# Performance work log

Measured on AMD Instinct MI355X. Metric: run time of the kernel, lower is better.

The kernel has to match this reference:

```python
import jax, jax.numpy as jnp
import numpy as np

CUTOFF = 10.0
NUM_GAUSSIANS = 50
LOG2 = float(np.log(2.0))
PI = float(np.pi)


def ssp(v):
    # shifted softplus: softplus(x) - log(2)
    return jax.nn.softplus(v) - LOG2


def setup_inputs() -> dict:
    key = jax.random.key(0)
    ks = jax.random.split(key, 16)
    N, E, H, F, G, L = 10000, 320000, 128, 128, NUM_GAUSSIANS, 6
    s = 0.08  # param scale to keep activations stable over 6 layers
    return {
        "x": jax.random.randint(ks[0], (N,), 0, 100),
        "edge_index": jax.random.randint(ks[1], (2, E), 0, N),
        "edge_dist": jax.random.uniform(ks[2], (E,), jnp.float32) * CUTOFF,
        "emb": jax.random.normal(ks[3], (100, H), jnp.float32) * s,
        "mlp_w1": jax.random.normal(ks[4], (L, G, F), jnp.float32) * s,
        "mlp_b1": jnp.zeros((L, F), jnp.float32),
        "mlp_w2": jax.random.normal(ks[5], (L, F, F), jnp.float32) * s,
        "mlp_b2": jnp.zeros((L, F), jnp.float32),
        "lin1_w": jax.random.normal(ks[6], (L, H, F), jnp.float32) * s,
        "lin2_w": jax.random.normal(ks[7], (L, F, H), jnp.float32) * s,
        "lin2_b": jnp.zeros((L, H), jnp.float32),
        "lin_w": jax.random.normal(ks[8], (L, H, H), jnp.float32) * s,
        "lin_b": jnp.zeros((L, H), jnp.float32),
        "out1_w": jax.random.normal(ks[9], (H, H // 2), jnp.float32) * s,
        "out1_b": jnp.zeros((H // 2,), jnp.float32),
        "out2_w": jax.random.normal(ks[10], (H // 2, H // 2), jnp.float32) * s,
        "out2_b": jnp.zeros((H // 2,), jnp.float32),
        "ro_w": jax.random.normal(ks[11], (H // 2, 12), jnp.float32) * s,
        "ro_b": jnp.zeros((12,), jnp.float32),
    }


def reference(x, edge_index, edge_dist, emb, mlp_w1, mlp_b1, mlp_w2, mlp_b2,
              lin1_w, lin2_w, lin2_b, lin_w, lin_b,
              out1_w, out1_b, out2_w, out2_b, ro_w, ro_b):
    N = x.shape[0]
    L = mlp_w1.shape[0]
    src, dst = edge_index[0], edge_index[1]

    h = emb[x]  # [N, H]

    # Gaussian smearing of distances -> [E, G]
    offset = jnp.linspace(0.0, CUTOFF, NUM_GAUSSIANS)
    coeff = -0.5 / (offset[1] - offset[0]) ** 2
    ea = jnp.exp(coeff * (edge_dist[:, None] - offset[None, :]) ** 2)

    # cosine cutoff envelope C [E]
    C = 0.5 * (jnp.cos(edge_dist * PI / CUTOFF) + 1.0)

    for l in range(L):
        # per-edge filter: MLP(gaussian) * cutoff  -> [E, F]
        W = (ssp(ea @ mlp_w1[l] + mlp_b1[l]) @ mlp_w2[l] + mlp_b2[l]) * C[:, None]
        xf = h @ lin1_w[l]                      # [N, F] (lin1, no bias)
        msg = xf[src] * W                       # gather + elementwise [E, F]
        agg = jax.ops.segment_sum(msg, dst, num_segments=N)  # scatter-add
        conv = agg @ lin2_w[l] + lin2_b[l]      # [N, H]
        h = h + (ssp(conv) @ lin_w[l] + lin_b[l])

    t = ssp(h @ out1_w + out1_b)
    t = t @ out2_w + out2_b
    h_agg = jnp.sum(t, axis=0)                  # [H//2]
    return h_agg @ ro_w + ro_b                  # [12]
```

## Files before the change

### kernel.cpp

```cpp
#include <hip/hip_runtime.h>
#include <math.h>

#define E_NUM 320000
#define N_NUM 10000
#define NB8   (N_NUM / 8)
#define NB16  (N_NUM / 16)
#define TAB   4096

typedef unsigned short ushort_t;
typedef short short8_t __attribute__((ext_vector_type(8)));
typedef float f32x4    __attribute__((ext_vector_type(4)));

#define WP_O1   294912
#define WP_O2   303104
#define WP_W1T  307200
#define WP_W2T  356352
#define WP_TOT  454656

__device__ __forceinline__ float ssp_f(float x) {
    return fmaxf(x, 0.f) + __logf(1.f + __expf(-fabsf(x))) - 0.69314718056f;
}

__device__ __forceinline__ float bf2f(ushort_t u) {
    union { unsigned int i; float f; } v;
    v.i = ((unsigned int)u) << 16;
    return v.f;
}
__device__ __forceinline__ ushort_t f2bf(float f) {
    union { float f; unsigned int i; } v;
    v.f = f;
    unsigned int u = v.i;
    unsigned int r = (u + 0x7FFFu + ((u >> 16) & 1u)) >> 16;
    return (ushort_t)r;
}

__global__ __launch_bounds__(256) void hist_kernel(const int* __restrict__ ei,
                                                   int* __restrict__ counts) {
    int e = blockIdx.x * 256 + threadIdx.x;
    if (e < E_NUM) atomicAdd(&counts[ei[E_NUM + e]], 1);
}

__global__ __launch_bounds__(256) void scan_kernel(const int* __restrict__ counts,
                                                   int* __restrict__ offs,
                                                   int* __restrict__ cursor) {
    __shared__ int part[256];
    const int tid = threadIdx.x;
    const int CH = 40;
    int base = tid * CH;
    int s = 0;
    for (int i = 0; i < CH; ++i) {
        int idx = base + i;
        if (idx < N_NUM) s += counts[idx];
    }
    part[tid] = s;
    __syncthreads();
    for (int off = 1; off < 256; off <<= 1) {
        int v = (tid >= off) ? part[tid - off] : 0;
        __syncthreads();
        part[tid] += v;
        __syncthreads();
    }
    int run = (tid > 0) ? part[tid - 1] : 0;
    for (int i = 0; i < CH; ++i) {
        int idx = base + i;
        if (idx < N_NUM) {
            offs[idx] = run;
            cursor[idx] = run;
            run += counts[idx];
        }
    }
    if (tid == 255) offs[N_NUM] = part[255];
}

__global__ __launch_bounds__(256) void scatter_kernel(const int* __restrict__ ei,
                                                      const float* __restrict__ dist,
                                                      int* __restrict__ cursor,
                                                      int* __restrict__ meta) {
    int e = blockIdx.x * 256 + threadIdx.x;
    if (e >= E_NUM) return;
    int d = ei[E_NUM + e];
    int pos = atomicAdd(&cursor[d], 1);
    float t = dist[e] * ((float)(TAB - 1) / 10.0f);
    int i0 = (int)(t + 0.5f);
    if (i0 > TAB - 1) i0 = TAB - 1;
    meta[pos] = (i0 << 14) | ei[e];
}

__global__ __launch_bounds__(256) void pack_kernel(const float* __restrict__ lin2_w,
                                                   const float* __restrict__ lin_w,
                                                   const float* __restrict__ lin1_w,
                                                   const float* __restrict__ o1w,
                                                   const float* __restrict__ o2w,
                                                   const float* __restrict__ mlp_w1,
                                                   const float* __restrict__ mlp_w2,
                                                   short* __restrict__ wpack) {
    int idx = blockIdx.x * 256 + threadIdx.x;
    const int M128 = 16384;
    if (idx < 18 * M128) {
        int g = idx / M128, r = idx % M128;
        const float* src;
        if (g < 6) src = lin2_w + g * M128;
        else if (g < 12) src = lin_w + (g - 6) * M128;
        else src = lin1_w + (g - 12) * M128;
        int j = r & 7, L = (r >> 3) & 63, ks = (r >> 9) & 3, t = r >> 11;
        int n = t * 16 + (L & 15);
        int k = ks * 32 + (L >> 4) * 8 + j;
        wpack[idx] = (short)f2bf(src[k * 128 + n]);
    } else if (idx < WP_O2) {
        int r = idx - WP_O1;
        int j = r & 7, L = (r >> 3) & 63, ks = (r >> 9) & 3, t = r >> 11;
        int n = t * 16 + (L & 15);
        int k = ks * 32 + (L >> 4) * 8 + j;
        wpack[idx] = (short)f2bf(o1w[k * 64 + n]);
    } else if (idx < WP_W1T) {
        int r = idx - WP_O2;
        int j = r & 7, L = (r >> 3) & 63, ks = (r >> 9) & 1, t = r >> 10;
        int n = t * 16 + (L & 15);
        int k = ks * 32 + (L >> 4) * 8 + j;
        wpack[idx] = (short)f2bf(o2w[k * 64 + n]);
    } else if (idx < WP_W2T) {
        int r2 = idx - WP_W1T;
        int g = r2 / 8192, r = r2 % 8192;
        int j = r & 7, L = (r >> 3) & 63, ks = (r >> 9) & 1, t = r >> 10;
        int n = t * 16 + (L & 15);
        int k = ks * 32 + (L >> 4) * 8 + j;
        float v = (k < 50) ? mlp_w1[g * 6400 + k * 128 + n] : 0.f;
        wpack[idx] = (short)f2bf(v);
    } else if (idx < WP_TOT) {
        int r2 = idx - WP_W2T;
        int g = r2 / M128, r = r2 % M128;
        int j = r & 7, L = (r >> 3) & 63, ks = (r >> 9) & 3, t = r >> 11;
        int n = t * 16 + (L & 15);
        int k = ks * 32 + (L >> 4) * 8 + j;
        wpack[idx] = (short)f2bf(mlp_w2[g * M128 + k * 128 + n]);
    }
}

__global__ __launch_bounds__(512) void table_kernel(const short* __restrict__ w1t,
                                                    const float* __restrict__ mlp_b1,
                                                    const short* __restrict__ w2t,
                                                    const float* __restrict__ mlp_b2,
                                                    ushort_t* __restrict__ tabB) {
    __shared__ short EA[16 * 72];
    __shared__ short HD[16 * 136];
    const int tid = threadIdx.x;
    const int wv = tid >> 6;
    const int lane = tid & 63;
    const int l = blockIdx.x >> 8;
    const int r0 = (blockIdx.x & 255) * 16;
    const float DG = 10.0f / (float)(TAB - 1);
    const float STEP = 10.0f / 49.0f;
    const float COEFF = -0.5f / (STEP * STEP);

    for (int i = tid; i < 16 * 64; i += 512) {
        int r = i >> 6, k = i & 63;
        float v = 0.f;
        if (k < 50) {
            float d = (float)(r0 + r) * DG;
            float t = d - (float)k * STEP;
            v = __expf(COEFF * t * t);
        }
        EA[r * 72 + k] = (short)f2bf(v);
    }
    __syncthreads();

    const int m = lane & 15, q = lane >> 4;

    {
        f32x4 acc = {0.f, 0.f, 0.f, 0.f};
        #pragma unroll
        for (int ks = 0; ks < 2; ++ks) {
            short8_t a = *(const short8_t*)(EA + m * 72 + ks * 32 + q * 8);
            short8_t b = *(const short8_t*)(w1t + l * 8192 + (wv * 2 + ks) * 512 + lane * 8);
            acc = __builtin_amdgcn_mfma_f32_16x16x32_bf16(a, b, acc, 0, 0, 0);
        }
        float bv = mlp_b1[l * 128 + wv * 16 + m];
        #pragma unroll
        for (int i = 0; i < 4; ++i)
            HD[(q * 4 + i) * 136 + wv * 16 + m] = (short)f2bf(ssp_f(acc[i] + bv));
    }
    __syncthreads();

    {
        f32x4 acc = {0.f, 0.f, 0.f, 0.f};
        #pragma unroll
        for (int ks = 0; ks < 4; ++ks) {
            short8_t a = *(const short8_t*)(HD + m * 136 + ks * 32 + q * 8);
            short8_t b = *(const short8_t*)(w2t + l * 16384 + (wv * 4 + ks) * 512 + lane * 8);
            acc = __builtin_amdgcn_mfma_f32_16x16x32_bf16(a, b, acc, 0, 0, 0);
        }
        int col = wv * 16 + m;
        float bv = mlp_b2[l * 128 + col];
        ushort_t* tl = tabB + (size_t)l * TAB * 128;
        #pragma unroll
        for (int i = 0; i < 4; ++i) {
            int row = r0 + q * 4 + i;
            float d = (float)row * DG;
            float C = 0.5f * (__cosf(d * 0.31415926535f) + 1.0f);
            tl[(size_t)row * 128 + col] = f2bf((acc[i] + bv) * C);
        }
    }
}

__device__ __forceinline__ void nacc(ushort4 x, ushort4 t,
                                     float& o0, float& o1, float& o2, float& o3) {
    o0 = fmaf(bf2f(x.x), bf2f(t.x), o0);
    o1 = fmaf(bf2f(x.y), bf2f(t.y), o1);
    o2 = fmaf(bf2f(x.z), bf2f(t.z), o2);
    o3 = fmaf(bf2f(x.w), bf2f(t.w), o3);
}

__global__ __launch_bounds__(256) void embed_lin1_kernel(const int* __restrict__ x,
                                                         const float* __restrict__ emb,
                                                         const float* __restrict__ B,
                                                         float* __restrict__ h,
                                                         ushort_t* __restrict__ xf) {
    __shared__ float AT[128][9];
    __shared__ int s_x[8];
    const int tid = threadIdx.x;
    const int n0 = blockIdx.x * 8;

    if (tid < 8) s_x[tid] = x[n0 + tid];
    __syncthreads();
    for (int i = tid; i < 8 * 128; i += 256) {
        int r = i >> 7, c = i & 127;
        float v = emb[s_x[r] * 128 + c];
        AT[c][r] = v;
        h[(size_t)(n0 + r) * 128 + c] = v;
    }
    __syncthreads();

    const int r  = tid & 7;
    const int c0 = (tid >> 3) * 4;
    float acc[4] = {0.f, 0.f, 0.f, 0.f};
    for (int k = 0; k < 128; k += 4) {
        float a[4];
        #pragma unroll
        for (int u = 0; u < 4; ++u) a[u] = AT[k + u][r];
        #pragma unroll
        for (int u = 0; u < 4; ++u) {
            float4 b = *(const float4*)(B + (size_t)(k + u) * 128 + c0);
            acc[0] = fmaf(a[u], b.x, acc[0]);
            acc[1] = fmaf(a[u], b.y, acc[1]);
            acc[2] = fmaf(a[u], b.z, acc[2]);
            acc[3] = fmaf(a[u], b.w, acc[3]);
        }
    }
    ushort4 o;
    o.x = f2bf(acc[0]); o.y = f2bf(acc[1]); o.z = f2bf(acc[2]); o.w = f2bf(acc[3]);
    *(ushort4*)(xf + (size_t)(n0 + r) * 128 + c0) = o;
}

template <bool LAST>
__global__ __launch_bounds__(512) void layer_kernel(const int* __restrict__ offs,
                                                    const int* __restrict__ meta,
                                                    const ushort_t* __restrict__ xf,
                                                    const ushort_t* __restrict__ tabB,
                                                    const short* __restrict__ w2p,
                                                    const float* __restrict__ lin2_b,
                                                    const short* __restrict__ wlp,
                                                    const float* __restrict__ lin_b,
                                                    const short* __restrict__ w1p,
                                                    float* __restrict__ h,
                                                    ushort_t* __restrict__ xf_out,
                                                    const short* __restrict__ o1p,
                                                    const float* __restrict__ o1b,
                                                    const short* __restrict__ o2p,
                                                    const float* __restrict__ o2b,
                                                    float* __restrict__ gs) {
    __shared__ short A1[16 * 136];
    __shared__ short A2[16 * 136];
    __shared__ float red[4][64];
    const int tid = threadIdx.x;
    const int n0 = blockIdx.x * 16;
    const int wv = tid >> 6;
    const int lane = tid & 63;

    {
        const int half = lane >> 5;
        const int c4 = (lane & 31) * 4;
        const int node = n0 + wv * 2 + half;
        int e   = offs[node];
        int end = offs[node + 1];

        float a0 = 0.f, a1 = 0.f, a2 = 0.f, a3 = 0.f;
        float b0 = 0.f, b1 = 0.f, b2 = 0.f, b3 = 0.f;

        for (; e + 8 <= end; e += 8) {
            int m[8];
            #pragma unroll
            for (int u = 0; u < 8; ++u) m[u] = meta[e + u];
            ushort4 xv[8], tv[8];
            #pragma unroll
            for (int u = 0; u < 8; ++u) {
                xv[u] = *(const ushort4*)(xf + (size_t)(m[u] & 0x3FFF) * 128 + c4);
                tv[u] = *(const ushort4*)(tabB + (size_t)((unsigned)m[u] >> 14) * 128 + c4);
            }
            nacc(xv[0], tv[0], a0, a1, a2, a3);
            nacc(xv[1], tv[1], b0, b1, b2, b3);
            nacc(xv[2], tv[2], a0, a1, a2, a3);
            nacc(xv[3], tv[3], b0, b1, b2, b3);
            nacc(xv[4], tv[4], a0, a1, a2, a3);
            nacc(xv[5], tv[5], b0, b1, b2, b3);
            nacc(xv[6], tv[6], a0, a1, a2, a3);
            nacc(xv[7], tv[7], b0, b1, b2, b3);
        }
        for (; e + 4 <= end; e += 4) {
            int m[4];
            #pragma unroll
            for (int u = 0; u < 4; ++u) m[u] = meta[e + u];
            ushort4 xv[4], tv[4];
            #pragma unroll
            for (int u = 0; u < 4; ++u) {
                xv[u] = *(const ushort4*)(xf + (size_t)(m[u] & 0x3FFF) * 128 + c4);
                tv[u] = *(const ushort4*)(tabB + (size_t)((unsigned)m[u] >> 14) * 128 + c4);
            }
            nacc(xv[0], tv[0], a0, a1, a2, a3);
            nacc(xv[1], tv[1], b0, b1, b2, b3);
            nacc(xv[2], tv[2], a0, a1, a2, a3);
            nacc(xv[3], tv[3], b0, b1, b2, b3);
        }
        for (; e < end; ++e) {
            int mm = meta[e];
            ushort4 xv = *(const ushort4*)(xf + (size_t)(mm & 0x3FFF) * 128 + c4);
            ushort4 tv = *(const ushort4*)(tabB + (size_t)((unsigned)mm >> 14) * 128 + c4);
            nacc(xv, tv, a0, a1, a2, a3);
        }

        unsigned p01 = (unsigned)f2bf(a0 + b0) | ((unsigned)f2bf(a1 + b1) << 16);
        unsigned p23 = (unsigned)f2bf(a2 + b2) | ((unsigned)f2bf(a3 + b3) << 16);
        const int row = wv * 2 + half;
        *(unsigned*)&A1[row * 136 + c4]     = p01;
        *(unsigned*)&A1[row * 136 + c4 + 2] = p23;
    }
    __syncthreads();

    const int m = lane & 15, q = lane >> 4;

    {
        f32x4 acc = {0.f, 0.f, 0.f, 0.f};
        #pragma unroll
        for (int ks = 0; ks < 4; ++ks) {
            short8_t a = *(const short8_t*)(A1 + m * 136 + ks * 32 + q * 8);
            short8_t b = *(const short8_t*)(w2p + (wv * 4 + ks) * 512 + lane * 8);
            acc = __builtin_amdgcn_mfma_f32_16x16x32_bf16(a, b, acc, 0, 0, 0);
        }
        float bv = lin2_b[wv * 16 + m];
        #pragma unroll
        for (int i = 0; i < 4; ++i) {
            int r = q * 4 + i;
            A2[r * 136 + wv * 16 + m] = (short)f2bf(ssp_f(acc[i] + bv));
        }
    }
    __syncthreads();

    {
        f32x4 acc = {0.f, 0.f, 0.f, 0.f};
        #pragma unroll
        for (int ks = 0; ks < 4; ++ks) {
            short8_t a = *(const short8_t*)(A2 + m * 136 + ks * 32 + q * 8);
            short8_t b = *(const short8_t*)(wlp + (wv * 4 + ks) * 512 + lane * 8);
            acc = __builtin_amdgcn_mfma_f32_16x16x32_bf16(a, b, acc, 0, 0, 0);
        }
        float bv = lin_b[wv * 16 + m];
        #pragma unroll
        for (int i = 0; i < 4; ++i) {
            int r = q * 4 + i;
            int grow = n0 + r;
            float h0 = h[(size_t)grow * 128 + wv * 16 + m];
            float hn = h0 + acc[i] + bv;
            if (!LAST) h[(size_t)grow * 128 + wv * 16 + m] = hn;
            A1[r * 136 + wv * 16 + m] = (short)f2bf(hn);
        }
    }
    __syncthreads();

    if constexpr (!LAST) {
        f32x4 acc = {0.f, 0.f, 0.f, 0.f};
        #pragma unroll
        for (int ks = 0; ks < 4; ++ks) {
            short8_t a = *(const short8_t*)(A1 + m * 136 + ks * 32 + q * 8);
            short8_t b = *(const short8_t*)(w1p + (wv * 4 + ks) * 512 + lane * 8);
            acc = __builtin_amdgcn_mfma_f32_16x16x32_bf16(a, b, acc, 0, 0, 0);
        }
        #pragma unroll
        for (int i = 0; i < 4; ++i) {
            int r = q * 4 + i;
            int grow = n0 + r;
            xf_out[(size_t)grow * 128 + wv * 16 + m] = f2bf(acc[i]);
        }
    } else {
        if (wv < 4) {
            f32x4 acc = {0.f, 0.f, 0.f, 0.f};
            #pragma unroll
            for (int ks = 0; ks < 4; ++ks) {
                short8_t a = *(const short8_t*)(A1 + m * 136 + ks * 32 + q * 8);
                short8_t b = *(const short8_t*)(o1p + (wv * 4 + ks) * 512 + lane * 8);
                acc = __builtin_amdgcn_mfma_f32_16x16x32_bf16(a, b, acc, 0, 0, 0);
            }
            float bv = o1b[wv * 16 + m];
            #pragma unroll
            for (int i = 0; i < 4; ++i) {
                int r = q * 4 + i;
                A2[r * 136 + wv * 16 + m] = (short)f2bf(ssp_f(acc[i] + bv));
            }
        }
        __syncthreads();
        if (wv < 4) {
            f32x4 acc = {0.f, 0.f, 0.f, 0.f};
            #pragma unroll
            for (int ks = 0; ks < 2; ++ks) {
                short8_t a = *(const short8_t*)(A2 + m * 136 + ks * 32 + q * 8);
                short8_t b = *(const short8_t*)(o2p + (wv * 2 + ks) * 512 + lane * 8);
                acc = __builtin_amdgcn_mfma_f32_16x16x32_bf16(a, b, acc, 0, 0, 0);
            }
            float bv = o2b[wv * 16 + m];
            float part = acc[0] + acc[1] + acc[2] + acc[3] + 4.0f * bv;
            red[q][wv * 16 + m] = part;
        }
        __syncthreads();
        if (tid < 64) {
            float s = red[0][tid] + red[1][tid] + red[2][tid] + red[3][tid];
            atomicAdd(&gs[tid], s);
        }
    }
}

__global__ void final_kernel(const float* __restrict__ gs,
                             const float* __restrict__ ro_w,
                             const float* __restrict__ ro_b,
                             float* __restrict__ out) {
    int i = threadIdx.x;
    if (i < 12) {
        float s = ro_b[i];
        for (int k = 0; k < 64; ++k) s = fmaf(gs[k], ro_w[k * 12 + i], s);
        out[i] = s;
    }
}

extern "C" void kernel_launch(void* const* d_in, const int* in_sizes, int n_in,
                              void* d_out, int out_size, void* d_ws, size_t ws_size,
                              hipStream_t stream) {
    const int*   x      = (const int*)d_in[0];
    const int*   ei     = (const int*)d_in[1];
    const float* dist   = (const float*)d_in[2];
    const float* emb    = (const float*)d_in[3];
    const float* mlp_w1 = (const float*)d_in[4];
    const float* mlp_b1 = (const float*)d_in[5];
    const float* mlp_w2 = (const float*)d_in[6];
    const float* mlp_b2 = (const float*)d_in[7];
    const float* lin1_w = (const float*)d_in[8];
    const float* lin2_w = (const float*)d_in[9];
    const float* lin2_b = (const float*)d_in[10];
    const float* lin_w  = (const float*)d_in[11];
    const float* lin_b  = (const float*)d_in[12];
    const float* out1_w = (const float*)d_in[13];
    const float* out1_b = (const float*)d_in[14];
    const float* out2_w = (const float*)d_in[15];
    const float* out2_b = (const float*)d_in[16];
    const float* ro_w   = (const float*)d_in[17];
    const float* ro_b   = (const float*)d_in[18];
    float* out = (float*)d_out;

    char* base = (char*)d_ws;
    float*    h     = (float*)base;     base += (size_t)N_NUM * 128 * 4;
    ushort_t* tabB  = (ushort_t*)base;  base += (size_t)6 * TAB * 128 * 2;
    ushort_t* xf0   = (ushort_t*)base;  base += (size_t)N_NUM * 128 * 2;
    ushort_t* xf1   = (ushort_t*)base;  base += (size_t)N_NUM * 128 * 2;
    int*      meta  = (int*)base;       base += (size_t)E_NUM * 4;
    short*    wpack = (short*)base;     base += (size_t)WP_TOT * 2;
    float*    gs    = (float*)base;     base += 64 * 4;
    int*      offs  = (int*)base;       base += (N_NUM + 1) * 4;
    int*      cursor= (int*)base;       base += N_NUM * 4;
    int*      counts= (int*)base;       base += N_NUM * 4;

    hipMemsetAsync(counts, 0, N_NUM * sizeof(int), stream);
    hipMemsetAsync(gs, 0, 64 * sizeof(float), stream);

    hist_kernel<<<(E_NUM + 255) / 256, 256, 0, stream>>>(ei, counts);
    scan_kernel<<<1, 256, 0, stream>>>(counts, offs, cursor);
    scatter_kernel<<<(E_NUM + 255) / 256, 256, 0, stream>>>(ei, dist, cursor, meta);

    pack_kernel<<<(WP_TOT + 255) / 256, 256, 0, stream>>>(
        lin2_w, lin_w, lin1_w, out1_w, out2_w, mlp_w1, mlp_w2, wpack);
    table_kernel<<<6 * (TAB / 16), 512, 0, stream>>>(
        wpack + WP_W1T, mlp_b1, wpack + WP_W2T, mlp_b2, tabB);

    embed_lin1_kernel<<<NB8, 256, 0, stream>>>(x, emb, lin1_w, h, xf0);

    const short* o1p = wpack + WP_O1;
    const short* o2p = wpack + WP_O2;

    for (int l = 0; l < 6; ++l) {
        ushort_t* xin  = (l & 1) ? xf1 : xf0;
        ushort_t* xout = (l & 1) ? xf0 : xf1;
        const ushort_t* tl = tabB + (size_t)l * TAB * 128;
        const short* w2p = wpack + l * 16384;
        const short* wlp = wpack + (6 + l) * 16384;
        if (l < 5) {
            const short* w1p = wpack + (12 + l + 1) * 16384;
            layer_kernel<false><<<NB16, 512, 0, stream>>>(
                offs, meta, xin, tl,
                w2p, lin2_b + l * 128, wlp, lin_b + l * 128, w1p,
                h, xout, nullptr, nullptr, nullptr, nullptr, nullptr);
        } else {
            layer_kernel<true><<<NB16, 512, 0, stream>>>(
                offs, meta, xin, tl,
                w2p, lin2_b + l * 128, wlp, lin_b + l * 128, nullptr,
                h, nullptr, o1p, out1_b, o2p, out2_b, gs);
        }
    }

    final_kernel<<<1, 64, 0, stream>>>(gs, ro_w, ro_b, out);
}
```

Baseline: 352.5 us.

## Halve layer block size, widen gather loads to 16B, shrink filter table

The layer kernel now runs with 256 threads per block. In the gather phase each 16-lane group handles one node with 8-element (16-byte) loads instead of 32 lanes with 4-element loads. Each wave now computes two 16-column tiles in the MFMA stages, so the 4 waves still cover all 128 columns. The filter lookup table is also halved to 2048 distance entries, which reduces table build work and cache footprint but coarsens the distance quantisation, and the meta index encoding must still fit.

```diff
diff --git a/kernel.cpp b/kernel.cpp
--- a/kernel.cpp
+++ b/kernel.cpp
@@ -5,7 +5,7 @@
 #define N_NUM 10000
 #define NB8   (N_NUM / 8)
 #define NB16  (N_NUM / 16)
-#define TAB   4096
+#define TAB   2048
 
 typedef unsigned short ushort_t;
 typedef short short8_t __attribute__((ext_vector_type(8)));
@@ -146,8 +146,8 @@
     const int tid = threadIdx.x;
     const int wv = tid >> 6;
     const int lane = tid & 63;
-    const int l = blockIdx.x >> 8;
-    const int r0 = (blockIdx.x & 255) * 16;
+    const int l = blockIdx.x >> 7;
+    const int r0 = (blockIdx.x & 127) * 16;
     const float DG = 10.0f / (float)(TAB - 1);
     const float STEP = 10.0f / 49.0f;
     const float COEFF = -0.5f / (STEP * STEP);
@@ -202,12 +202,10 @@
     }
 }
 
-__device__ __forceinline__ void nacc(ushort4 x, ushort4 t,
-                                     float& o0, float& o1, float& o2, float& o3) {
-    o0 = fmaf(bf2f(x.x), bf2f(t.x), o0);
-    o1 = fmaf(bf2f(x.y), bf2f(t.y), o1);
-    o2 = fmaf(bf2f(x.z), bf2f(t.z), o2);
-    o3 = fmaf(bf2f(x.w), bf2f(t.w), o3);
+__device__ __forceinline__ void nacc8(short8_t x, short8_t t, float* o) {
+    #pragma unroll
+    for (int j = 0; j < 8; ++j)
+        o[j] = fmaf(bf2f((ushort_t)x[j]), bf2f((ushort_t)t[j]), o[j]);
 }
 
 __global__ __launch_bounds__(256) void embed_lin1_kernel(const int* __restrict__ x,
@@ -251,8 +249,22 @@
     *(ushort4*)(xf + (size_t)(n0 + r) * 128 + c0) = o;
 }
 
+__device__ __forceinline__ void mfma_stage2(const short* A_lds, const short* wp,
+                                            int lane, int t0, int t1,
+                                            f32x4& acc0, f32x4& acc1) {
+    const int m = lane & 15, q = lane >> 4;
+    #pragma unroll
+    for (int ks = 0; ks < 4; ++ks) {
+        short8_t a  = *(const short8_t*)(A_lds + m * 136 + ks * 32 + q * 8);
+        short8_t b0 = *(const short8_t*)(wp + (t0 * 4 + ks) * 512 + lane * 8);
+        short8_t b1 = *(const short8_t*)(wp + (t1 * 4 + ks) * 512 + lane * 8);
+        acc0 = __builtin_amdgcn_mfma_f32_16x16x32_bf16(a, b0, acc0, 0, 0, 0);
+        acc1 = __builtin_amdgcn_mfma_f32_16x16x32_bf16(a, b1, acc1, 0, 0, 0);
+    }
+}
+
 template <bool LAST>
-__global__ __launch_bounds__(512) void layer_kernel(const int* __restrict__ offs,
+__global__ __launch_bounds__(256) void layer_kernel(const int* __restrict__ offs,
                                                     const int* __restrict__ meta,
                                                     const ushort_t* __restrict__ xf,
                                                     const ushort_t* __restrict__ tabB,
@@ -277,120 +289,109 @@
     const int lane = tid & 63;
 
     {
-        const int half = lane >> 5;
-        const int c4 = (lane & 31) * 4;
-        const int node = n0 + wv * 2 + half;
+        const int qt = lane >> 4;
+        const int c8 = (lane & 15) * 8;
+        const int node = n0 + wv * 4 + qt;
         int e   = offs[node];
         int end = offs[node + 1];
 
-        float a0 = 0.f, a1 = 0.f, a2 = 0.f, a3 = 0.f;
-        float b0 = 0.f, b1 = 0.f, b2 = 0.f, b3 = 0.f;
+        float accA[8] = {0.f, 0.f, 0.f, 0.f, 0.f, 0.f, 0.f, 0.f};
+        float accB[8] = {0.f, 0.f, 0.f, 0.f, 0.f, 0.f, 0.f, 0.f};
 
         for (; e + 8 <= end; e += 8) {
             int m[8];
             #pragma unroll
             for (int u = 0; u < 8; ++u) m[u] = meta[e + u];
-            ushort4 xv[8], tv[8];
+            short8_t xv[8], tv[8];
             #pragma unroll
             for (int u = 0; u < 8; ++u) {
-                xv[u] = *(const ushort4*)(xf + (size_t)(m[u] & 0x3FFF) * 128 + c4);
-                tv[u] = *(const ushort4*)(tabB + (size_t)((unsigned)m[u] >> 14) * 128 + c4);
+                xv[u] = *(const short8_t*)(xf + (size_t)(m[u] & 0x3FFF) * 128 + c8);
+                tv[u] = *(const short8_t*)(tabB + (size_t)((unsigned)m[u] >> 14) * 128 + c8);
             }
-            nacc(xv[0], tv[0], a0, a1, a2, a3);
-            nacc(xv[1], tv[1], b0, b1, b2, b3);
-            nacc(xv[2], tv[2], a0, a1, a2, a3);
-            nacc(xv[3], tv[3], b0, b1, b2, b3);
-            nacc(xv[4], tv[4], a0, a1, a2, a3);
-            nacc(xv[5], tv[5], b0, b1, b2, b3);
-            nacc(xv[6], tv[6], a0, a1, a2, a3);
-            nacc(xv[7], tv[7], b0, b1, b2, b3);
+            #pragma unroll
+            for (int u = 0; u < 8; ++u)
+                nacc8(xv[u], tv[u], (u & 1) ? accB : accA);
         }
         for (; e + 4 <= end; e += 4) {
             int m[4];
             #pragma unroll
             for (int u = 0; u < 4; ++u) m[u] = meta[e + u];
-            ushort4 xv[4], tv[4];
+            short8_t xv[4], tv[4];
             #pragma unroll
             for (int u = 0; u < 4; ++u) {
-                xv[u] = *(const ushort4*)(xf + (size_t)(m[u] & 0x3FFF) * 128 + c4);
-                tv[u] = *(const ushort4*)(tabB + (size_t)((unsigned)m[u] >> 14) * 128 + c4);
+                xv[u] = *(const short8_t*)(xf + (size_t)(m[u] & 0x3FFF) * 128 + c8);
+                tv[u] = *(const short8_t*)(tabB + (size_t)((unsigned)m[u] >> 14) * 128 + c8);
             }
-            nacc(xv[0], tv[0], a0, a1, a2, a3);
-            nacc(xv[1], tv[1], b0, b1, b2, b3);
-            nacc(xv[2], tv[2], a0, a1, a2, a3);
-            nacc(xv[3], tv[3], b0, b1, b2, b3);
+            #pragma unroll
+            for (int u = 0; u < 4; ++u)
+                nacc8(xv[u], tv[u], (u & 1) ? accB : accA);
         }
         for (; e < end; ++e) {
             int mm = meta[e];
-            ushort4 xv = *(const ushort4*)(xf + (size_t)(mm & 0x3FFF) * 128 + c4);
-            ushort4 tv = *(const ushort4*)(tabB + (size_t)((unsigned)mm >> 14) * 128 + c4);
-            nacc(xv, tv, a0, a1, a2, a3);
-        }
-
-        unsigned p01 = (unsigned)f2bf(a0 + b0) | ((unsigned)f2bf(a1 + b1) << 16);
-        unsigned p23 = (unsigned)f2bf(a2 + b2) | ((unsigned)f2bf(a3 + b3) << 16);
-        const int row = wv * 2 + half;
-        *(unsigned*)&A1[row * 136 + c4]     = p01;
-        *(unsigned*)&A1[row * 136 + c4 + 2] = p23;
+            short8_t xv = *(const short8_t*)(xf + (size_t)(mm & 0x3FFF) * 128 + c8);
+            short8_t tv = *(const short8_t*)(tabB + (size_t)((unsigned)mm >> 14) * 128 + c8);
+            nacc8(xv, tv, accA);
+        }
+
+        short8_t out;
+        #pragma unroll
+        for (int j = 0; j < 8; ++j) out[j] = (short)f2bf(accA[j] + accB[j]);
+        *(short8_t*)&A1[(wv * 4 + qt) * 136 + c8] = out;
     }
     __syncthreads();
 
     const int m = lane & 15, q = lane >> 4;
+    const int t0 = wv * 2, t1 = wv * 2 + 1;
 
     {
-        f32x4 acc = {0.f, 0.f, 0.f, 0.f};
-        #pragma unroll
-        for (int ks = 0; ks < 4; ++ks) {
-            short8_t a = *(const short8_t*)(A1 + m * 136 + ks * 32 + q * 8);
-            short8_t b = *(const short8_t*)(w2p + (wv * 4 + ks) * 512 + lane * 8);
-            acc = __builtin_amdgcn_mfma_f32_16x16x32_bf16(a, b, acc, 0, 0, 0);
-        }
-        float bv = lin2_b[wv * 16 + m];
+        f32x4 acc0 = {0.f, 0.f, 0.f, 0.f}, acc1 = {0.f, 0.f, 0.f, 0.f};
+        mfma_stage2(A1, w2p, lane, t0, t1, acc0, acc1);
+        float bv0 = lin2_b[t0 * 16 + m];
+        float bv1 = lin2_b[t1 * 16 + m];
         #pragma unroll
         for (int i = 0; i < 4; ++i) {
             int r = q * 4 + i;
-            A2[r * 136 + wv * 16 + m] = (short)f2bf(ssp_f(acc[i] + bv));
+            A2[r * 136 + t0 * 16 + m] = (short)f2bf(ssp_f(acc0[i] + bv0));
+            A2[r * 136 + t1 * 16 + m] = (short)f2bf(ssp_f(acc1[i] + bv1));
         }
     }
     __syncthreads();
 
     {
-        f32x4 acc = {0.f, 0.f, 0.f, 0.f};
-        #pragma unroll
-        for (int ks = 0; ks < 4; ++ks) {
-            short8_t a = *(const short8_t*)(A2 + m * 136 + ks * 32 + q * 8);
-            short8_t b = *(const short8_t*)(wlp + (wv * 4 + ks) * 512 + lane * 8);
-            acc = __builtin_amdgcn_mfma_f32_16x16x32_bf16(a, b, acc, 0, 0, 0);
-        }
-        float bv = lin_b[wv * 16 + m];
+        f32x4 acc0 = {0.f, 0.f, 0.f, 0.f}, acc1 = {0.f, 0.f, 0.f, 0.f};
+        mfma_stage2(A2, wlp, lane, t0, t1, acc0, acc1);
+        float bv0 = lin_b[t0 * 16 + m];
+        float bv1 = lin_b[t1 * 16 + m];
         #pragma unroll
         for (int i = 0; i < 4; ++i) {
             int r = q * 4 + i;
             int grow = n0 + r;
-            float h0 = h[(size_t)grow * 128 + wv * 16 + m];
-            float hn = h0 + acc[i] + bv;
-            if (!LAST) h[(size_t)grow * 128 + wv * 16 + m] = hn;
-            A1[r * 136 + wv * 16 + m] = (short)f2bf(hn);
+            float h0 = h[(size_t)grow * 128 + t0 * 16 + m];
+            float h1 = h[(size_t)grow * 128 + t1 * 16 + m];
+            float hn0 = h0 + acc0[i] + bv0;
+            float hn1 = h1 + acc1[i] + bv1;
+            if (!LAST) {
+                h[(size_t)grow * 128 + t0 * 16 + m] = hn0;
+                h[(size_t)grow * 128 + t1 * 16 + m] = hn1;
+            }
+            A1[r * 136 + t0 * 16 + m] = (short)f2bf(hn0);
+            A1[r * 136 + t1 * 16 + m] = (short)f2bf(hn1);
         }
     }
     __syncthreads();
 
     if constexpr (!LAST) {
-        f32x4 acc = {0.f, 0.f, 0.f, 0.f};
-        #pragma unroll
-        for (int ks = 0; ks < 4; ++ks) {
-            short8_t a = *(const short8_t*)(A1 + m * 136 + ks * 32 + q * 8);
-            short8_t b = *(const short8_t*)(w1p + (wv * 4 + ks) * 512 + lane * 8);
-            acc = __builtin_amdgcn_mfma_f32_16x16x32_bf16(a, b, acc, 0, 0, 0);
-        }
+        f32x4 acc0 = {0.f, 0.f, 0.f, 0.f}, acc1 = {0.f, 0.f, 0.f, 0.f};
+        mfma_stage2(A1, w1p, lane, t0, t1, acc0, acc1);
         #pragma unroll
         for (int i = 0; i < 4; ++i) {
             int r = q * 4 + i;
             int grow = n0 + r;
-            xf_out[(size_t)grow * 128 + wv * 16 + m] = f2bf(acc[i]);
+            xf_out[(size_t)grow * 128 + t0 * 16 + m] = f2bf(acc0[i]);
+            xf_out[(size_t)grow * 128 + t1 * 16 + m] = f2bf(acc1[i]);
         }
     } else {
-        if (wv < 4) {
+        {
             f32x4 acc = {0.f, 0.f, 0.f, 0.f};
             #pragma unroll
             for (int ks = 0; ks < 4; ++ks) {
@@ -406,7 +407,7 @@
             }
         }
         __syncthreads();
-        if (wv < 4) {
+        {
             f32x4 acc = {0.f, 0.f, 0.f, 0.f};
             #pragma unroll
             for (int ks = 0; ks < 2; ++ks) {
@@ -499,12 +500,12 @@
         const short* wlp = wpack + (6 + l) * 16384;
         if (l < 5) {
             const short* w1p = wpack + (12 + l + 1) * 16384;
-            layer_kernel<false><<<NB16, 512, 0, stream>>>(
+            layer_kernel<false><<<NB16, 256, 0, stream>>>(
                 offs, meta, xin, tl,
                 w2p, lin2_b + l * 128, wlp, lin_b + l * 128, w1p,
                 h, xout, nullptr, nullptr, nullptr, nullptr, nullptr);
         } else {
-            layer_kernel<true><<<NB16, 512, 0, stream>>>(
+            layer_kernel<true><<<NB16, 256, 0, stream>>>(
                 offs, meta, xin, tl,
                 w2p, lin2_b + l * 128, wlp, lin_b + l * 128, nullptr,
                 h, nullptr, o1p, out1_b, o2p, out2_b, gs);
```

Result: faster. 320.4 us, median of 2 (-9.1%).

## Split each node's edges across two 16-lane groups with 16-byte gathers

Applied to the files above, without the earlier changes.

The edge aggregation now assigns four nodes' halves per wave. Each 16-lane group loads 8 bf16 values per lane (16-byte loads) over half of a node's edge range, and the two partial sums are combined through a shared-memory float buffer. This doubles the independent gather streams per wave and widens each load, which should raise memory-level parallelism in the latency-bound gather. The cost is an extra LDS buffer and an extra synchronisation. Separately, the distance lookup table is halved from 4096 to 2048 entries, which coarsens the filter resolution but shrinks the table's cache footprint and halves the table-building work.

```diff
diff --git a/kernel.cpp b/kernel.cpp
--- a/kernel.cpp
+++ b/kernel.cpp
@@ -5,7 +5,7 @@
 #define N_NUM 10000
 #define NB8   (N_NUM / 8)
 #define NB16  (N_NUM / 16)
-#define TAB   4096
+#define TAB   2048
 
 typedef unsigned short ushort_t;
 typedef short short8_t __attribute__((ext_vector_type(8)));
@@ -146,8 +146,8 @@
     const int tid = threadIdx.x;
     const int wv = tid >> 6;
     const int lane = tid & 63;
-    const int l = blockIdx.x >> 8;
-    const int r0 = (blockIdx.x & 255) * 16;
+    const int l = blockIdx.x >> 7;
+    const int r0 = (blockIdx.x & 127) * 16;
     const float DG = 10.0f / (float)(TAB - 1);
     const float STEP = 10.0f / 49.0f;
     const float COEFF = -0.5f / (STEP * STEP);
@@ -202,12 +202,10 @@
     }
 }
 
-__device__ __forceinline__ void nacc(ushort4 x, ushort4 t,
-                                     float& o0, float& o1, float& o2, float& o3) {
-    o0 = fmaf(bf2f(x.x), bf2f(t.x), o0);
-    o1 = fmaf(bf2f(x.y), bf2f(t.y), o1);
-    o2 = fmaf(bf2f(x.z), bf2f(t.z), o2);
-    o3 = fmaf(bf2f(x.w), bf2f(t.w), o3);
+__device__ __forceinline__ void nacc8(short8_t x, short8_t t, float* o) {
+    #pragma unroll
+    for (int j = 0; j < 8; ++j)
+        o[j] = fmaf(bf2f((ushort_t)x[j]), bf2f((ushort_t)t[j]), o[j]);
 }
 
 __global__ __launch_bounds__(256) void embed_lin1_kernel(const int* __restrict__ x,
@@ -270,6 +268,7 @@
                                                     float* __restrict__ gs) {
     __shared__ short A1[16 * 136];
     __shared__ short A2[16 * 136];
+    __shared__ float PF[32][132];
     __shared__ float red[4][64];
     const int tid = threadIdx.x;
     const int n0 = blockIdx.x * 16;
@@ -277,61 +276,67 @@
     const int lane = tid & 63;
 
     {
-        const int half = lane >> 5;
-        const int c4 = (lane & 31) * 4;
-        const int node = n0 + wv * 2 + half;
-        int e   = offs[node];
-        int end = offs[node + 1];
-
-        float a0 = 0.f, a1 = 0.f, a2 = 0.f, a3 = 0.f;
-        float b0 = 0.f, b1 = 0.f, b2 = 0.f, b3 = 0.f;
-
-        for (; e + 8 <= end; e += 8) {
+        const int qt = lane >> 4;
+        const int c8 = (lane & 15) * 8;
+        const int s = wv * 4 + qt;
+        const int node = n0 + (s >> 1);
+        const int half = s & 1;
+        int beg = offs[node], end = offs[node + 1];
+        int mid = beg + ((end - beg) >> 1);
+        int e    = half ? mid : beg;
+        int stop = half ? end : mid;
+
+        float accA[8] = {0.f, 0.f, 0.f, 0.f, 0.f, 0.f, 0.f, 0.f};
+        float accB[8] = {0.f, 0.f, 0.f, 0.f, 0.f, 0.f, 0.f, 0.f};
+
+        for (; e + 8 <= stop; e += 8) {
             int m[8];
             #pragma unroll
             for (int u = 0; u < 8; ++u) m[u] = meta[e + u];
-            ushort4 xv[8], tv[8];
+            short8_t xv[8], tv[8];
             #pragma unroll
             for (int u = 0; u < 8; ++u) {
-                xv[u] = *(const ushort4*)(xf + (size_t)(m[u] & 0x3FFF) * 128 + c4);
-                tv[u] = *(const ushort4*)(tabB + (size_t)((unsigned)m[u] >> 14) * 128 + c4);
+                xv[u] = *(const short8_t*)(xf + (size_t)(m[u] & 0x3FFF) * 128 + c8);
+                tv[u] = *(const short8_t*)(tabB + (size_t)((unsigned)m[u] >> 14) * 128 + c8);
             }
-            nacc(xv[0], tv[0], a0, a1, a2, a3);
-            nacc(xv[1], tv[1], b0, b1, b2, b3);
-            nacc(xv[2], tv[2], a0, a1, a2, a3);
-            nacc(xv[3], tv[3], b0, b1, b2, b3);
-            nacc(xv[4], tv[4], a0, a1, a2, a3);
-            nacc(xv[5], tv[5], b0, b1, b2, b3);
-            nacc(xv[6], tv[6], a0, a1, a2, a3);
-            nacc(xv[7], tv[7], b0, b1, b2, b3);
-        }
-        for (; e + 4 <= end; e += 4) {
+            #pragma unroll
+            for (int u = 0; u < 8; ++u)
+                nacc8(xv[u], tv[u], (u & 1) ? accB : accA);
+        }
+        for (; e + 4 <= stop; e += 4) {
             int m[4];
             #pragma unroll
             for (int u = 0; u < 4; ++u) m[u] = meta[e + u];
-            ushort4 xv[4], tv[4];
+            short8_t xv[4], tv[4];
             #pragma unroll
             for (int u = 0; u < 4; ++u) {
-                xv[u] = *(const ushort4*)(xf + (size_t)(m[u] & 0x3FFF) * 128 + c4);
-                tv[u] = *(const ushort4*)(tabB + (size_t)((unsigned)m[u] >> 14) * 128 + c4);
+                xv[u] = *(const short8_t*)(xf + (size_t)(m[u] & 0x3FFF) * 128 + c8);
+                tv[u] = *(const short8_t*)(tabB + (size_t)((unsigned)m[u] >> 14) * 128 + c8);
             }
-            nacc(xv[0], tv[0], a0, a1, a2, a3);
-            nacc(xv[1], tv[1], b0, b1, b2, b3);
-            nacc(xv[2], tv[2], a0, a1, a2, a3);
-            nacc(xv[3], tv[3], b0, b1, b2, b3);
-        }
-        for (; e < end; ++e) {
+            #pragma unroll
+            for (int u = 0; u < 4; ++u)
+                nacc8(xv[u], tv[u], (u & 1) ? accB : accA);
+        }
+        for (; e < stop; ++e) {
             int mm = meta[e];
-            ushort4 xv = *(const ushort4*)(xf + (size_t)(mm & 0x3FFF) * 128 + c4);
-            ushort4 tv = *(const ushort4*)(tabB + (size_t)((unsigned)mm >> 14) * 128 + c4);
-            nacc(xv, tv, a0, a1, a2, a3);
-        }
-
-        unsigned p01 = (unsigned)f2bf(a0 + b0) | ((unsigned)f2bf(a1 + b1) << 16);
-        unsigned p23 = (unsigned)f2bf(a2 + b2) | ((unsigned)f2bf(a3 + b3) << 16);
-        const int row = wv * 2 + half;
-        *(unsigned*)&A1[row * 136 + c4]     = p01;
-        *(unsigned*)&A1[row * 136 + c4 + 2] = p23;
+            short8_t xv = *(const short8_t*)(xf + (size_t)(mm & 0x3FFF) * 128 + c8);
+            short8_t tv = *(const short8_t*)(tabB + (size_t)((unsigned)mm >> 14) * 128 + c8);
+            nacc8(xv, tv, accA);
+        }
+
+        float4 p0, p1;
+        p0.x = accA[0] + accB[0]; p0.y = accA[1] + accB[1];
+        p0.z = accA[2] + accB[2]; p0.w = accA[3] + accB[3];
+        p1.x = accA[4] + accB[4]; p1.y = accA[5] + accB[5];
+        p1.z = accA[6] + accB[6]; p1.w = accA[7] + accB[7];
+        *(float4*)&PF[s][c8]     = p0;
+        *(float4*)&PF[s][c8 + 4] = p1;
+    }
+    __syncthreads();
+
+    for (int idx = tid; idx < 16 * 128; idx += 512) {
+        int r = idx >> 7, c = idx & 127;
+        A1[r * 136 + c] = (short)f2bf(PF[2 * r][c] + PF[2 * r + 1][c]);
     }
     __syncthreads();
 
```

New measurement: 336.2 us. -4.6%, faster.
